# Kernel optimization log

Measured on AMD Instinct MI355X. Metric: run time of the kernel, lower is better.

Reference implementation:

```python
import jax, jax.numpy as jnp
import numpy as np

ALPHA = 0.2  # LeakyReLU negative slope
NEG_INF = -9e15


def _xavier(key, shape, gain=1.414):
    fan_in, fan_out = shape[-2], shape[-1]
    lim = gain * np.sqrt(6.0 / (fan_in + fan_out))
    return jax.random.uniform(key, shape, jnp.float32, -lim, lim)


def setup_inputs() -> dict:
    key = jax.random.key(0)
    ks = jax.random.split(key, 8)
    B, N, Din, H, Dh, Do = 8, 1024, 256, 4, 128, 64
    x = jax.random.normal(ks[0], (B, N, Din), jnp.float32)
    adj = jax.random.randint(ks[1], (B, N, N), 0, 2).astype(jnp.int32)
    W_heads = _xavier(ks[2], (H, Din, Dh))                 # per-head W
    a_heads = _xavier(ks[3], (H, 2 * Dh, 1))[..., 0]       # per-head a, [H, 2*Dh]
    W_out = _xavier(ks[4], (H * Dh, Do))                   # out_att W
    a_out = _xavier(ks[5], (2 * Do, 1))[..., 0]            # out_att a, [2*Do]
    Wf = _xavier(ks[6], (Do, Do), gain=1.0)                # fc_out linear
    bf = jnp.zeros((Do,), jnp.float32)
    return {"x": x, "adj": adj, "W_heads": W_heads, "a_heads": a_heads,
            "W_out": W_out, "a_out": a_out, "Wf": Wf, "bf": bf}


def _leaky_relu(v):
    return jnp.where(v >= 0, v, ALPHA * v)


def _gat(h, adj, W, a):
    # h: [B,N,Fin], adj: [B,N,N], W: [Fin,Fout], a: [2*Fout]
    Wh = h @ W                                   # [B,N,F]
    F = W.shape[-1]
    # additive attention: e_ij = leakyrelu(a_src.Wh_i + a_dst.Wh_j)
    src = Wh @ a[:F]                             # [B,N]
    dst = Wh @ a[F:]                             # [B,N]
    e = _leaky_relu(src[:, :, None] + dst[:, None, :])   # [B,N,N]
    scores = jnp.where(adj > 0, e, NEG_INF)
    attn = jax.nn.softmax(scores, axis=-1)       # dropout is a no-op in eval
    return attn @ Wh                             # [B,N,F]


def reference(x, adj, W_heads, a_heads, W_out, a_out, Wf, bf):
    B, N, _ = x.shape
    H, _, Dh = W_heads.shape
    # multi-head GAT, heads vmapped over leading axis of W_heads / a_heads
    heads = jax.vmap(_gat, in_axes=(None, None, 0, 0))(x, adj, W_heads, a_heads)  # [H,B,N,Dh]
    xcat = jnp.moveaxis(heads, 0, 2).reshape(B, N, H * Dh)   # concat heads, dim=2
    out = jax.nn.elu(_gat(xcat, adj, W_out, a_out))           # [B,N,Do]
    out = jax.nn.relu(out @ Wf + bf)                          # fc_out (dropout no-op)
    return out
```

## Files before the change

kernel.cpp:

```cpp
#include <hip/hip_runtime.h>
#include <hip/hip_bf16.h>

#define BSZ 8
#define NN 1024
#define DIN 256
#define NH 4
#define DH 128
#define DOUT 64
#define RTOT (BSZ*NN)
#define FCAT (NH*DH)
#define ALPHA 0.2f

typedef unsigned short ushortT;
typedef __attribute__((ext_vector_type(8))) short bf16x8;
typedef __attribute__((ext_vector_type(4))) float f32x4;

static __device__ __forceinline__ ushortT f2bf(float f) {
    __hip_bfloat16 h = __float2bfloat16(f);
    return *reinterpret_cast<ushortT*>(&h);
}
static __device__ __forceinline__ float bfu2f(ushortT u) {
    return __uint_as_float(((unsigned)u) << 16);
}
static __device__ __forceinline__ void split2(float v, ushortT& hi, ushortT& lo) {
    hi = f2bf(v);
    lo = f2bf(v - bfu2f(hi));
}
static __device__ __forceinline__ void gload16(const ushortT* g, ushortT* l) {
    __builtin_amdgcn_global_load_lds(
        (const __attribute__((address_space(1))) unsigned int*)(const void*)g,
        (__attribute__((address_space(3))) unsigned int*)(void*)l, 16, 0, 0);
}

__global__ __launch_bounds__(256) void k_prepw(const float* __restrict__ W,
                                               const float* __restrict__ Wout,
                                               ushortT* __restrict__ WbTh, ushortT* __restrict__ WbTl,
                                               ushortT* __restrict__ WoTh, ushortT* __restrict__ WoTl) {
    const int g2 = blockIdx.x * 256 + threadIdx.x;
    if (g2 < NH * DH * DIN) {
        const int h = g2 >> 15, f = (g2 >> 8) & 127, k = g2 & 255;
        const int kt = k >> 6, k64 = k & 63;
        const float v = W[(size_t)h * DIN * DH + (size_t)k * DH + f];
        ushortT hi, lo; split2(v, hi, lo);
        const int idx = ((h * 4 + kt) * 128 + f) * 64 + k64;
        WbTh[idx] = hi; WbTl[idx] = lo;
    } else {
        const int g3 = g2 - NH * DH * DIN;
        const int f = g3 >> 9, k = g3 & 511;
        const float v = Wout[(size_t)k * DOUT + f];
        ushortT hi, lo; split2(v, hi, lo);
        WoTh[g3] = hi; WoTl[g3] = lo;
    }
}

__global__ __launch_bounds__(512) void k_main(const float* __restrict__ x,
                                              const float* __restrict__ ah_,
                                              const ushortT* __restrict__ WbTh,
                                              const ushortT* __restrict__ WbTl,
                                              const int* __restrict__ adj,
                                              unsigned* __restrict__ adjbit,
                                              ushortT* __restrict__ WhT,
                                              float* __restrict__ src1,
                                              float* __restrict__ dst1) {
    __shared__ ushortT Ah[128 * 64], Al[128 * 64];
    __shared__ ushortT Bh[128 * 64], Bl[128 * 64];
    __shared__ float sred[8][32], dred[8][32];
    const int tid = threadIdx.x;
    if (blockIdx.x >= 256) {
        const int g = (blockIdx.x - 256) * 512 + tid;
        const int row = g >> 5, w = g & 31;
        const int4* p = (const int4*)(adj + (size_t)row * NN + w * 32);
        unsigned m = 0;
#pragma unroll
        for (int q = 0; q < 8; ++q) {
            const int4 v = p[q];
            m |= (v.x > 0 ? 1u : 0u) << (q * 4 + 0);
            m |= (v.y > 0 ? 1u : 0u) << (q * 4 + 1);
            m |= (v.z > 0 ? 1u : 0u) << (q * 4 + 2);
            m |= (v.w > 0 ? 1u : 0u) << (q * 4 + 3);
        }
        adjbit[g] = m;
        return;
    }
    const int lane = tid & 63, wave = tid >> 6;
    const int h = blockIdx.x >> 6, mt = blockIdx.x & 63;
    const int r0 = mt * 128, b = r0 >> 10, jr = r0 & 1023;
    const int m16 = lane & 15, quad = lane >> 4;
    const int mg = wave >> 1, fg = wave & 1;
    const int arow = tid >> 2, apart = tid & 3;
    f32x4 acc[2][4];
#pragma unroll
    for (int a = 0; a < 2; ++a)
#pragma unroll
        for (int c = 0; c < 4; ++c) acc[a][c] = (f32x4){0.f, 0.f, 0.f, 0.f};

    for (int kt = 0; kt < 4; ++kt) {
        __syncthreads();
        const ushortT* planeH = WbTh + (size_t)((h * 4 + kt) * 128) * 64;
        const ushortT* planeL = WbTl + (size_t)((h * 4 + kt) * 128) * 64;
#pragma unroll
        for (int half = 0; half < 2; ++half) {
            const int f = wave * 16 + half * 8 + (lane >> 3);
            const int sc = (lane & 7) ^ (f & 7);
            gload16(planeH + (size_t)f * 64 + sc * 8, Bh + (wave * 16 + half * 8) * 64);
            gload16(planeL + (size_t)f * 64 + sc * 8, Bl + (wave * 16 + half * 8) * 64);
        }
        {
            const float4* xs = (const float4*)(x + (size_t)(r0 + arow) * DIN + kt * 64 + apart * 16);
            union { ushortT u[16]; uint4 q[2]; } th, tl;
#pragma unroll
            for (int e = 0; e < 4; ++e) {
                const float4 v = xs[e];
                split2(v.x, th.u[e * 4 + 0], tl.u[e * 4 + 0]);
                split2(v.y, th.u[e * 4 + 1], tl.u[e * 4 + 1]);
                split2(v.z, th.u[e * 4 + 2], tl.u[e * 4 + 2]);
                split2(v.w, th.u[e * 4 + 3], tl.u[e * 4 + 3]);
            }
            const int s0 = (2 * apart) ^ (arow & 7), s1 = (2 * apart + 1) ^ (arow & 7);
            *(uint4*)&Ah[arow * 64 + s0 * 8] = th.q[0];
            *(uint4*)&Ah[arow * 64 + s1 * 8] = th.q[1];
            *(uint4*)&Al[arow * 64 + s0 * 8] = tl.q[0];
            *(uint4*)&Al[arow * 64 + s1 * 8] = tl.q[1];
        }
        __syncthreads();
#pragma unroll
        for (int ks = 0; ks < 2; ++ks) {
            bf16x8 a_h[2], a_l[2], b_h[4], b_l[4];
#pragma unroll
            for (int ms = 0; ms < 2; ++ms) {
                const int row = (mg * 2 + ms) * 16 + m16;
                const int cl = (ks * 4 + quad) ^ (row & 7);
                a_h[ms] = *(const bf16x8*)&Ah[row * 64 + cl * 8];
                a_l[ms] = *(const bf16x8*)&Al[row * 64 + cl * 8];
            }
#pragma unroll
            for (int fs = 0; fs < 4; ++fs) {
                const int row = (fg * 4 + fs) * 16 + m16;
                const int cl = (ks * 4 + quad) ^ (row & 7);
                b_h[fs] = *(const bf16x8*)&Bh[row * 64 + cl * 8];
                b_l[fs] = *(const bf16x8*)&Bl[row * 64 + cl * 8];
            }
#pragma unroll
            for (int ms = 0; ms < 2; ++ms)
#pragma unroll
                for (int fs = 0; fs < 4; ++fs) {
                    acc[ms][fs] = __builtin_amdgcn_mfma_f32_16x16x32_bf16(a_h[ms], b_h[fs], acc[ms][fs], 0, 0, 0);
                    acc[ms][fs] = __builtin_amdgcn_mfma_f32_16x16x32_bf16(a_h[ms], b_l[fs], acc[ms][fs], 0, 0, 0);
                    acc[ms][fs] = __builtin_amdgcn_mfma_f32_16x16x32_bf16(a_l[ms], b_h[fs], acc[ms][fs], 0, 0, 0);
                }
        }
    }
    float sacc[2][4] = {{0,0,0,0},{0,0,0,0}}, dacc[2][4] = {{0,0,0,0},{0,0,0,0}};
#pragma unroll
    for (int ms = 0; ms < 2; ++ms)
#pragma unroll
        for (int fs = 0; fs < 4; ++fs) {
            const int fl = (fg * 4 + fs) * 16 + m16;
            const float a_s = ah_[h * 2 * DH + fl];
            const float a_d = ah_[h * 2 * DH + DH + fl];
            union { ushortT u[4]; uint2 q; } tw;
#pragma unroll
            for (int reg = 0; reg < 4; ++reg) {
                const float v = acc[ms][fs][reg];
                sacc[ms][reg] += v * a_s;
                dacc[ms][reg] += v * a_d;
                tw.u[reg] = f2bf(v);
            }
            *(uint2*)(WhT + ((size_t)((b * NH + h) * DH + fl)) * NN + jr + (mg * 2 + ms) * 16 + quad * 4) = tw.q;
        }
#pragma unroll
    for (int ms = 0; ms < 2; ++ms) {
#pragma unroll
        for (int reg = 0; reg < 4; ++reg) {
            float s = sacc[ms][reg], d = dacc[ms][reg];
#pragma unroll
            for (int o = 8; o > 0; o >>= 1) {
                s += __shfl_xor(s, o, 64);
                d += __shfl_xor(d, o, 64);
            }
            if (m16 == 0) {
                sred[wave][ms * 16 + quad * 4 + reg] = s;
                dred[wave][ms * 16 + quad * 4 + reg] = d;
            }
        }
    }
    __syncthreads();
    if (tid < 128) {
        const int mgr = tid >> 5, idx = tid & 31;
        src1[h * RTOT + r0 + tid] = sred[mgr * 2][idx] + sred[mgr * 2 + 1][idx];
        dst1[h * RTOT + r0 + tid] = dred[mgr * 2][idx] + dred[mgr * 2 + 1][idx];
    }
}

__global__ __launch_bounds__(256) void k_attn1(const unsigned* __restrict__ adjbit,
                                               const ushortT* __restrict__ WhT,
                                               const float* __restrict__ src1,
                                               const float* __restrict__ dst1,
                                               ushortT* __restrict__ xcat) {
    __shared__ ushortT As[32 * 64];
    __shared__ ushortT Bs[128 * 64];
    __shared__ unsigned maskS[32 * 32];
    __shared__ float dstv[NN];
    __shared__ float srcv[32], rowinv[32], red4[4];
    const int tid = threadIdx.x, lane = tid & 63, wave = tid >> 6;
    const int bh = blockIdx.x & 31, it = blockIdx.x >> 5;
    const int b = bh >> 2, h = bh & 3;
    const int i0 = it * 32;
    const int m16 = lane & 15, quad = lane >> 4;

    const unsigned* mbase = adjbit + (size_t)(b * NN + i0) * 32;
#pragma unroll
    for (int k2 = 0; k2 < 4; ++k2) maskS[tid + 256 * k2] = mbase[tid + 256 * k2];
    float lm = -INFINITY;
#pragma unroll
    for (int k2 = 0; k2 < 4; ++k2) {
        const float d = dst1[h * RTOT + b * NN + tid + 256 * k2];
        dstv[tid + 256 * k2] = d;
        lm = fmaxf(lm, d);
    }
    if (tid < 32) srcv[tid] = src1[h * RTOT + b * NN + i0 + tid];
#pragma unroll
    for (int o = 32; o > 0; o >>= 1) lm = fmaxf(lm, __shfl_xor(lm, o, 64));
    if (lane == 0) red4[wave] = lm;
    __syncthreads();
    const float dmax = fmaxf(fmaxf(red4[0], red4[1]), fmaxf(red4[2], red4[3]));

    const int arow = tid >> 3, apart = tid & 7;
    const float si = srcv[arow];
    float mrow = si + dmax;
    mrow = mrow >= 0.f ? mrow : ALPHA * mrow;
    float fsum = 0.f;

    const ushortT* Bbase = WhT + (size_t)(bh * DH) * NN;
    f32x4 acc[2][2];
#pragma unroll
    for (int a = 0; a < 2; ++a)
#pragma unroll
        for (int c = 0; c < 2; ++c) acc[a][c] = (f32x4){0.f, 0.f, 0.f, 0.f};

    for (int kt = 0; kt < 16; ++kt) {
        __syncthreads();
#pragma unroll
        for (int half = 0; half < 4; ++half) {
            const int f = wave * 32 + half * 8 + (lane >> 3);
            gload16(Bbase + (size_t)f * NN + kt * 64 + (((lane & 7) ^ (f & 7)) * 8),
                    Bs + (wave * 32 + half * 8) * 64);
        }
        {
            const unsigned w0 = maskS[arow * 32 + kt * 2 + (apart >> 2)];
            const int bb = (apart & 3) * 8;
            union { ushortT u[8]; uint4 q; } tw;
#pragma unroll
            for (int e4 = 0; e4 < 2; ++e4) {
                const float4 dv = *(const float4*)&dstv[kt * 64 + apart * 8 + e4 * 4];
                const float vv[4] = {dv.x, dv.y, dv.z, dv.w};
#pragma unroll
                for (int e = 0; e < 4; ++e) {
                    float v = si + vv[e];
                    v = v >= 0.f ? v : ALPHA * v;
                    const unsigned bit = (w0 >> (bb + e4 * 4 + e)) & 1u;
                    const float p = bit ? __expf(v - mrow) : 0.f;
                    fsum += p;
                    tw.u[e4 * 4 + e] = f2bf(p);
                }
            }
            *(uint4*)&As[arow * 64 + (apart ^ (arow & 7)) * 8] = tw.q;
        }
        __syncthreads();
#pragma unroll
        for (int ks = 0; ks < 2; ++ks) {
            bf16x8 afr[2];
#pragma unroll
            for (int ms = 0; ms < 2; ++ms) {
                const int rowa = ms * 16 + m16;
                const int cla = (ks * 4 + quad) ^ (rowa & 7);
                afr[ms] = *(const bf16x8*)&As[rowa * 64 + cla * 8];
            }
#pragma unroll
            for (int ff = 0; ff < 2; ++ff) {
                const int rowb = wave * 32 + ff * 16 + m16;
                const int clb = (ks * 4 + quad) ^ (rowb & 7);
                const bf16x8 bfr = *(const bf16x8*)&Bs[rowb * 64 + clb * 8];
#pragma unroll
                for (int ms = 0; ms < 2; ++ms)
                    acc[ms][ff] = __builtin_amdgcn_mfma_f32_16x16x32_bf16(afr[ms], bfr, acc[ms][ff], 0, 0, 0);
            }
        }
    }
#pragma unroll
    for (int o = 1; o < 8; o <<= 1) fsum += __shfl_xor(fsum, o, 64);
    if ((lane & 7) == 0) rowinv[arow] = 1.f / fsum;
    __syncthreads();
#pragma unroll
    for (int ms = 0; ms < 2; ++ms) {
        float rv[4];
#pragma unroll
        for (int reg = 0; reg < 4; ++reg) rv[reg] = rowinv[ms * 16 + quad * 4 + reg];
#pragma unroll
        for (int ff = 0; ff < 2; ++ff) {
            const int f = h * DH + wave * 32 + ff * 16 + m16;
#pragma unroll
            for (int reg = 0; reg < 4; ++reg) {
                const int i = i0 + ms * 16 + quad * 4 + reg;
                xcat[(size_t)(b * NN + i) * FCAT + f] = f2bf(acc[ms][ff][reg] * rv[reg]);
            }
        }
    }
}

__global__ __launch_bounds__(256) void k_wh2(const ushortT* __restrict__ xcat,
                                             const ushortT* __restrict__ WoTh,
                                             const ushortT* __restrict__ WoTl,
                                             const float* __restrict__ aout,
                                             ushortT* __restrict__ Wh2T,
                                             float* __restrict__ src2,
                                             float* __restrict__ dst2) {
    __shared__ ushortT As[32 * 64];
    __shared__ ushortT Bh[64 * 64], Bl[64 * 64];
    __shared__ float sred[4][16], dred[4][16];
    const int tid = threadIdx.x, lane = tid & 63, wave = tid >> 6;
    const int r0 = blockIdx.x * 32;
    const int b = r0 >> 10, jr = r0 & 1023;
    const int m16 = lane & 15, quad = lane >> 4;
    const int mg = wave >> 1, fg = wave & 1;
    f32x4 acc[2] = {(f32x4){0.f,0.f,0.f,0.f}, (f32x4){0.f,0.f,0.f,0.f}};

    for (int kt = 0; kt < 8; ++kt) {
        __syncthreads();
        {
            const int row = wave * 8 + (lane >> 3);
            const int sc = (lane & 7) ^ (row & 7);
            gload16(xcat + (size_t)(r0 + row) * FCAT + kt * 64 + sc * 8, As + wave * 8 * 64);
        }
#pragma unroll
        for (int half = 0; half < 2; ++half) {
            const int f = wave * 16 + half * 8 + (lane >> 3);
            const int sc = (lane & 7) ^ (f & 7);
            gload16(WoTh + (size_t)f * FCAT + kt * 64 + sc * 8, Bh + (wave * 16 + half * 8) * 64);
            gload16(WoTl + (size_t)f * FCAT + kt * 64 + sc * 8, Bl + (wave * 16 + half * 8) * 64);
        }
        __syncthreads();
#pragma unroll
        for (int ks = 0; ks < 2; ++ks) {
            const int rowa = mg * 16 + m16;
            const int cla = (ks * 4 + quad) ^ (rowa & 7);
            const bf16x8 afr = *(const bf16x8*)&As[rowa * 64 + cla * 8];
#pragma unroll
            for (int ff = 0; ff < 2; ++ff) {
                const int rowb = fg * 32 + ff * 16 + m16;
                const int clb = (ks * 4 + quad) ^ (rowb & 7);
                const bf16x8 b_h = *(const bf16x8*)&Bh[rowb * 64 + clb * 8];
                const bf16x8 b_l = *(const bf16x8*)&Bl[rowb * 64 + clb * 8];
                acc[ff] = __builtin_amdgcn_mfma_f32_16x16x32_bf16(afr, b_h, acc[ff], 0, 0, 0);
                acc[ff] = __builtin_amdgcn_mfma_f32_16x16x32_bf16(afr, b_l, acc[ff], 0, 0, 0);
            }
        }
    }
    float sv[4] = {0, 0, 0, 0}, dv[4] = {0, 0, 0, 0};
#pragma unroll
    for (int ff = 0; ff < 2; ++ff) {
        const int f = fg * 32 + ff * 16 + m16;
        const float a_s = aout[f], a_d = aout[DOUT + f];
        union { ushortT u[4]; uint2 q; } tw;
#pragma unroll
        for (int reg = 0; reg < 4; ++reg) {
            const float v = acc[ff][reg];
            sv[reg] += v * a_s;
            dv[reg] += v * a_d;
            tw.u[reg] = f2bf(v);
        }
        *(uint2*)(Wh2T + ((size_t)(b * DOUT + f)) * NN + jr + mg * 16 + quad * 4) = tw.q;
    }
#pragma unroll
    for (int reg = 0; reg < 4; ++reg) {
#pragma unroll
        for (int o = 8; o > 0; o >>= 1) {
            sv[reg] += __shfl_xor(sv[reg], o, 64);
            dv[reg] += __shfl_xor(dv[reg], o, 64);
        }
        if (m16 == 0) { sred[wave][quad * 4 + reg] = sv[reg]; dred[wave][quad * 4 + reg] = dv[reg]; }
    }
    __syncthreads();
    if (tid < 32) {
        const int mgr = tid >> 4, idx = tid & 15;
        src2[r0 + tid] = sred[mgr * 2][idx] + sred[mgr * 2 + 1][idx];
        dst2[r0 + tid] = dred[mgr * 2][idx] + dred[mgr * 2 + 1][idx];
    }
}

__global__ __launch_bounds__(256) void k_attn2(const unsigned* __restrict__ adjbit,
                                               const ushortT* __restrict__ Wh2T,
                                               const float* __restrict__ src2,
                                               const float* __restrict__ dst2,
                                               const float* __restrict__ Wf,
                                               const float* __restrict__ bfv,
                                               float* __restrict__ out) {
    __shared__ ushortT As[32 * 64];
    __shared__ ushortT Bs[64 * 64];
    __shared__ unsigned maskS[32 * 32];
    __shared__ float dstv[NN];
    __shared__ ushortT Wfh[64 * 64], Wfl[64 * 64];
    __shared__ float t2s[32 * 68];
    __shared__ float srcv[32], rowinv[32], red4[4];
    const int tid = threadIdx.x, lane = tid & 63, wave = tid >> 6;
    const int b = blockIdx.x & 7, it = blockIdx.x >> 3;
    const int i0 = it * 32;
    const int m16 = lane & 15, quad = lane >> 4;

    const unsigned* mbase = adjbit + (size_t)(b * NN + i0) * 32;
#pragma unroll
    for (int k2 = 0; k2 < 4; ++k2) maskS[tid + 256 * k2] = mbase[tid + 256 * k2];
    float lm = -INFINITY;
#pragma unroll
    for (int k2 = 0; k2 < 4; ++k2) {
        const float d = dst2[b * NN + tid + 256 * k2];
        dstv[tid + 256 * k2] = d;
        lm = fmaxf(lm, d);
    }
    if (tid < 32) srcv[tid] = src2[b * NN + i0 + tid];
    {
        const int c = tid & 63, kc = (tid >> 6) * 16;
        union { ushortT u[16]; uint4 q[2]; } th, tl;
#pragma unroll
        for (int e = 0; e < 16; ++e)
            split2(Wf[(size_t)(kc + e) * DOUT + c], th.u[e], tl.u[e]);
        const int s0 = ((tid >> 6) * 2) ^ (c & 7), s1 = ((tid >> 6) * 2 + 1) ^ (c & 7);
        *(uint4*)&Wfh[c * 64 + s0 * 8] = th.q[0];
        *(uint4*)&Wfh[c * 64 + s1 * 8] = th.q[1];
        *(uint4*)&Wfl[c * 64 + s0 * 8] = tl.q[0];
        *(uint4*)&Wfl[c * 64 + s1 * 8] = tl.q[1];
    }
#pragma unroll
    for (int o = 32; o > 0; o >>= 1) lm = fmaxf(lm, __shfl_xor(lm, o, 64));
    if (lane == 0) red4[wave] = lm;
    __syncthreads();
    const float dmax = fmaxf(fmaxf(red4[0], red4[1]), fmaxf(red4[2], red4[3]));

    const int arow = tid >> 3, apart = tid & 7;
    const float si = srcv[arow];
    float mrow = si + dmax;
    mrow = mrow >= 0.f ? mrow : ALPHA * mrow;
    float fsum = 0.f;

    const int mfrag = wave >> 1, fh = wave & 1;
    const ushortT* Bbase = Wh2T + (size_t)(b * DOUT) * NN;
    f32x4 acc[2] = {(f32x4){0.f,0.f,0.f,0.f}, (f32x4){0.f,0.f,0.f,0.f}};

    for (int kt = 0; kt < 16; ++kt) {
        __syncthreads();
#pragma unroll
        for (int half = 0; half < 2; ++half) {
            const int f = wave * 16 + half * 8 + (lane >> 3);
            gload16(Bbase + (size_t)f * NN + kt * 64 + (((lane & 7) ^ (f & 7)) * 8),
                    Bs + (wave * 16 + half * 8) * 64);
        }
        {
            const unsigned w0 = maskS[arow * 32 + kt * 2 + (apart >> 2)];
            const int bb = (apart & 3) * 8;
            union { ushortT u[8]; uint4 q; } tw;
#pragma unroll
            for (int e4 = 0; e4 < 2; ++e4) {
                const float4 dv = *(const float4*)&dstv[kt * 64 + apart * 8 + e4 * 4];
                const float vv[4] = {dv.x, dv.y, dv.z, dv.w};
#pragma unroll
                for (int e = 0; e < 4; ++e) {
                    float v = si + vv[e];
                    v = v >= 0.f ? v : ALPHA * v;
                    const unsigned bit = (w0 >> (bb + e4 * 4 + e)) & 1u;
                    const float p = bit ? __expf(v - mrow) : 0.f;
                    fsum += p;
                    tw.u[e4 * 4 + e] = f2bf(p);
                }
            }
            *(uint4*)&As[arow * 64 + (apart ^ (arow & 7)) * 8] = tw.q;
        }
        __syncthreads();
#pragma unroll
        for (int ks = 0; ks < 2; ++ks) {
            const int rowa = mfrag * 16 + m16;
            const int cla = (ks * 4 + quad) ^ (rowa & 7);
            const bf16x8 afr = *(const bf16x8*)&As[rowa * 64 + cla * 8];
#pragma unroll
            for (int ff = 0; ff < 2; ++ff) {
                const int rowb = (fh * 2 + ff) * 16 + m16;
                const int clb = (ks * 4 + quad) ^ (rowb & 7);
                const bf16x8 bfr = *(const bf16x8*)&Bs[rowb * 64 + clb * 8];
                acc[ff] = __builtin_amdgcn_mfma_f32_16x16x32_bf16(afr, bfr, acc[ff], 0, 0, 0);
            }
        }
    }
#pragma unroll
    for (int o = 1; o < 8; o <<= 1) fsum += __shfl_xor(fsum, o, 64);
    if ((lane & 7) == 0) rowinv[arow] = 1.f / fsum;
    __syncthreads();
#pragma unroll
    for (int ff = 0; ff < 2; ++ff) {
#pragma unroll
        for (int reg = 0; reg < 4; ++reg) {
            const int row = mfrag * 16 + quad * 4 + reg;
            float v = acc[ff][reg] * rowinv[row];
            v = v > 0.f ? v : (__expf(v) - 1.f);
            t2s[row * 68 + (fh * 2 + ff) * 16 + m16] = v;
        }
    }
    __syncthreads();
    const int mf = wave >> 1, nh = wave & 1;
    f32x4 oacc[2];
#pragma unroll
    for (int g = 0; g < 2; ++g) {
        const float bias = bfv[(nh * 2 + g) * 16 + m16];
        oacc[g] = (f32x4){bias, bias, bias, bias};
    }
#pragma unroll
    for (int ks = 0; ks < 2; ++ks) {
        const int rowa = mf * 16 + m16;
        const float4 fA = *(const float4*)&t2s[rowa * 68 + ks * 32 + quad * 8];
        const float4 fB = *(const float4*)&t2s[rowa * 68 + ks * 32 + quad * 8 + 4];
        union { ushortT u[8]; bf16x8 v; } a_h, a_l;
        const float av[8] = {fA.x, fA.y, fA.z, fA.w, fB.x, fB.y, fB.z, fB.w};
#pragma unroll
        for (int e = 0; e < 8; ++e) split2(av[e], a_h.u[e], a_l.u[e]);
#pragma unroll
        for (int g = 0; g < 2; ++g) {
            const int rowc = (nh * 2 + g) * 16 + m16;
            const int cl = (ks * 4 + quad) ^ (rowc & 7);
            const bf16x8 b_h = *(const bf16x8*)&Wfh[rowc * 64 + cl * 8];
            const bf16x8 b_l = *(const bf16x8*)&Wfl[rowc * 64 + cl * 8];
            oacc[g] = __builtin_amdgcn_mfma_f32_16x16x32_bf16(a_h.v, b_h, oacc[g], 0, 0, 0);
            oacc[g] = __builtin_amdgcn_mfma_f32_16x16x32_bf16(a_h.v, b_l, oacc[g], 0, 0, 0);
            oacc[g] = __builtin_amdgcn_mfma_f32_16x16x32_bf16(a_l.v, b_h, oacc[g], 0, 0, 0);
        }
    }
#pragma unroll
    for (int g = 0; g < 2; ++g) {
        const int c = (nh * 2 + g) * 16 + m16;
#pragma unroll
        for (int reg = 0; reg < 4; ++reg) {
            const int i = i0 + mf * 16 + quad * 4 + reg;
            out[(size_t)(b * NN + i) * DOUT + c] = fmaxf(oacc[g][reg], 0.f);
        }
    }
}

extern "C" void kernel_launch(void* const* d_in, const int* in_sizes, int n_in,
                              void* d_out, int out_size, void* d_ws, size_t ws_size,
                              hipStream_t stream) {
    const float* x   = (const float*)d_in[0];
    const int*   adj = (const int*)d_in[1];
    const float* Wh  = (const float*)d_in[2];
    const float* ah  = (const float*)d_in[3];
    const float* Wo  = (const float*)d_in[4];
    const float* ao  = (const float*)d_in[5];
    const float* Wf  = (const float*)d_in[6];
    const float* bf  = (const float*)d_in[7];
    float* out = (float*)d_out;

    float* ws    = (float*)d_ws;
    float* src1  = ws;
    float* dst1  = src1 + NH * RTOT;
    float* src2  = dst1 + NH * RTOT;
    float* dst2  = src2 + RTOT;
    ushortT* WhT   = (ushortT*)(dst2 + RTOT);
    ushortT* Wh2T  = WhT + (size_t)RTOT * FCAT;
    ushortT* xcat  = Wh2T + (size_t)RTOT * DOUT;
    ushortT* WbTh  = xcat + (size_t)RTOT * FCAT;
    ushortT* WbTl  = WbTh + NH * DH * DIN;
    ushortT* WoTh  = WbTl + NH * DH * DIN;
    ushortT* WoTl  = WoTh + DOUT * FCAT;
    unsigned* adjbit = (unsigned*)(WoTl + DOUT * FCAT);

    hipLaunchKernelGGL(k_prepw, dim3((NH * DH * DIN + DOUT * FCAT) / 256), dim3(256), 0, stream,
                       Wh, Wo, WbTh, WbTl, WoTh, WoTl);
    hipLaunchKernelGGL(k_main,  dim3(768), dim3(512), 0, stream,
                       x, ah, WbTh, WbTl, adj, adjbit, WhT, src1, dst1);
    hipLaunchKernelGGL(k_attn1, dim3(1024), dim3(256), 0, stream,
                       adjbit, WhT, src1, dst1, xcat);
    hipLaunchKernelGGL(k_wh2,   dim3(256), dim3(256), 0, stream,
                       xcat, WoTh, WoTl, ao, Wh2T, src2, dst2);
    hipLaunchKernelGGL(k_attn2, dim3(256), dim3(256), 0, stream,
                       adjbit, Wh2T, src2, dst2, Wf, bf, out);
}
```

Baseline: 158.6 us.

## Double-buffer attention tiles in k_attn1 to overlap staging with MFMA

Doubles the As and Bs shared-memory tiles in the first-layer attention kernel. The next tile's attention weights and WhT slice are now staged while the current tile runs its MFMAs, with one barrier per iteration instead of two. This aims to hide global-load latency and the exp/mask arithmetic behind matrix work. In exchange, LDS use per block roughly doubles for these tiles, which may lower occupancy. Correctness depends on the barrier also waiting for the asynchronous loads to finish.

```diff
diff --git a/kernel.cpp b/kernel.cpp
--- a/kernel.cpp
+++ b/kernel.cpp
@@ -197,8 +197,8 @@
                                                const float* __restrict__ src1,
                                                const float* __restrict__ dst1,
                                                ushortT* __restrict__ xcat) {
-    __shared__ ushortT As[32 * 64];
-    __shared__ ushortT Bs[128 * 64];
+    __shared__ ushortT As[2][32 * 64];
+    __shared__ ushortT Bs[2][128 * 64];
     __shared__ unsigned maskS[32 * 32];
     __shared__ float dstv[NN];
     __shared__ float srcv[32], rowinv[32], red4[4];
@@ -238,35 +238,41 @@
 #pragma unroll
         for (int c = 0; c < 2; ++c) acc[a][c] = (f32x4){0.f, 0.f, 0.f, 0.f};
 
+#define STAGE_TILE(kt_, buf_)                                                              \
+    {                                                                                      \
+        const int kt__ = (kt_);                                                            \
+        ushortT* bdst = &Bs[(buf_)][0];                                                    \
+        _Pragma("unroll")                                                                  \
+        for (int half = 0; half < 4; ++half) {                                             \
+            const int f = wave * 32 + half * 8 + (lane >> 3);                              \
+            gload16(Bbase + (size_t)f * NN + kt__ * 64 + (((lane & 7) ^ (f & 7)) * 8),     \
+                    bdst + (wave * 32 + half * 8) * 64);                                   \
+        }                                                                                  \
+        const unsigned w0 = maskS[arow * 32 + kt__ * 2 + (apart >> 2)];                    \
+        const int bb = (apart & 3) * 8;                                                    \
+        union { ushortT u[8]; uint4 q; } tw;                                               \
+        _Pragma("unroll")                                                                  \
+        for (int e4 = 0; e4 < 2; ++e4) {                                                   \
+            const float4 dv = *(const float4*)&dstv[kt__ * 64 + apart * 8 + e4 * 4];       \
+            const float vv[4] = {dv.x, dv.y, dv.z, dv.w};                                  \
+            _Pragma("unroll")                                                              \
+            for (int e = 0; e < 4; ++e) {                                                  \
+                float v = si + vv[e];                                                      \
+                v = v >= 0.f ? v : ALPHA * v;                                              \
+                const unsigned bit = (w0 >> (bb + e4 * 4 + e)) & 1u;                       \
+                const float p = bit ? __expf(v - mrow) : 0.f;                              \
+                fsum += p;                                                                 \
+                tw.u[e4 * 4 + e] = f2bf(p);                                                \
+            }                                                                              \
+        }                                                                                  \
+        *(uint4*)&As[(buf_)][arow * 64 + (apart ^ (arow & 7)) * 8] = tw.q;                 \
+    }
+
+    STAGE_TILE(0, 0);
     for (int kt = 0; kt < 16; ++kt) {
-        __syncthreads();
-#pragma unroll
-        for (int half = 0; half < 4; ++half) {
-            const int f = wave * 32 + half * 8 + (lane >> 3);
-            gload16(Bbase + (size_t)f * NN + kt * 64 + (((lane & 7) ^ (f & 7)) * 8),
-                    Bs + (wave * 32 + half * 8) * 64);
-        }
-        {
-            const unsigned w0 = maskS[arow * 32 + kt * 2 + (apart >> 2)];
-            const int bb = (apart & 3) * 8;
-            union { ushortT u[8]; uint4 q; } tw;
-#pragma unroll
-            for (int e4 = 0; e4 < 2; ++e4) {
-                const float4 dv = *(const float4*)&dstv[kt * 64 + apart * 8 + e4 * 4];
-                const float vv[4] = {dv.x, dv.y, dv.z, dv.w};
-#pragma unroll
-                for (int e = 0; e < 4; ++e) {
-                    float v = si + vv[e];
-                    v = v >= 0.f ? v : ALPHA * v;
-                    const unsigned bit = (w0 >> (bb + e4 * 4 + e)) & 1u;
-                    const float p = bit ? __expf(v - mrow) : 0.f;
-                    fsum += p;
-                    tw.u[e4 * 4 + e] = f2bf(p);
-                }
-            }
-            *(uint4*)&As[arow * 64 + (apart ^ (arow & 7)) * 8] = tw.q;
-        }
-        __syncthreads();
+        const int cb = kt & 1;
+        __syncthreads();
+        if (kt < 15) STAGE_TILE(kt + 1, cb ^ 1);
 #pragma unroll
         for (int ks = 0; ks < 2; ++ks) {
             bf16x8 afr[2];
@@ -274,19 +280,20 @@
             for (int ms = 0; ms < 2; ++ms) {
                 const int rowa = ms * 16 + m16;
                 const int cla = (ks * 4 + quad) ^ (rowa & 7);
-                afr[ms] = *(const bf16x8*)&As[rowa * 64 + cla * 8];
+                afr[ms] = *(const bf16x8*)&As[cb][rowa * 64 + cla * 8];
             }
 #pragma unroll
             for (int ff = 0; ff < 2; ++ff) {
                 const int rowb = wave * 32 + ff * 16 + m16;
                 const int clb = (ks * 4 + quad) ^ (rowb & 7);
-                const bf16x8 bfr = *(const bf16x8*)&Bs[rowb * 64 + clb * 8];
+                const bf16x8 bfr = *(const bf16x8*)&Bs[cb][rowb * 64 + clb * 8];
 #pragma unroll
                 for (int ms = 0; ms < 2; ++ms)
                     acc[ms][ff] = __builtin_amdgcn_mfma_f32_16x16x32_bf16(afr[ms], bfr, acc[ms][ff], 0, 0, 0);
             }
         }
     }
+#undef STAGE_TILE
 #pragma unroll
     for (int o = 1; o < 8; o <<= 1) fsum += __shfl_xor(fsum, o, 64);
     if ((lane & 7) == 0) rowinv[arow] = 1.f / fsum;
```

New measurement: 155.6 us (median of 2 runs). No clear change (-1.9%).

## Compute attention probabilities directly in MFMA A-fragment registers, drop LDS staging

Applied to the files above, without the earlier changes.

Each wave now owns 16 rows and 64 features, and builds its bf16 probability A-fragment in registers in the exact MFMA lane layout. This removes the As shared buffer, its store/load round trip, and the rowinv/srcv shared arrays; row sums are reduced with lane shuffles. In exchange, each exp is now computed by two waves (the 2 feature-half waves share rows), doubling exp work per block.

```diff
diff --git a/kernel.cpp b/kernel.cpp
--- a/kernel.cpp
+++ b/kernel.cpp
@@ -197,16 +197,16 @@
                                                const float* __restrict__ src1,
                                                const float* __restrict__ dst1,
                                                ushortT* __restrict__ xcat) {
-    __shared__ ushortT As[32 * 64];
     __shared__ ushortT Bs[128 * 64];
     __shared__ unsigned maskS[32 * 32];
     __shared__ float dstv[NN];
-    __shared__ float srcv[32], rowinv[32], red4[4];
+    __shared__ float red4[4];
     const int tid = threadIdx.x, lane = tid & 63, wave = tid >> 6;
     const int bh = blockIdx.x & 31, it = blockIdx.x >> 5;
     const int b = bh >> 2, h = bh & 3;
     const int i0 = it * 32;
     const int m16 = lane & 15, quad = lane >> 4;
+    const int rw = wave >> 1, fw = wave & 1;
 
     const unsigned* mbase = adjbit + (size_t)(b * NN + i0) * 32;
 #pragma unroll
@@ -218,25 +218,22 @@
         dstv[tid + 256 * k2] = d;
         lm = fmaxf(lm, d);
     }
-    if (tid < 32) srcv[tid] = src1[h * RTOT + b * NN + i0 + tid];
 #pragma unroll
     for (int o = 32; o > 0; o >>= 1) lm = fmaxf(lm, __shfl_xor(lm, o, 64));
     if (lane == 0) red4[wave] = lm;
     __syncthreads();
     const float dmax = fmaxf(fmaxf(red4[0], red4[1]), fmaxf(red4[2], red4[3]));
 
-    const int arow = tid >> 3, apart = tid & 7;
-    const float si = srcv[arow];
+    const int rloc = rw * 16 + m16;
+    const float si = src1[h * RTOT + b * NN + i0 + rloc];
     float mrow = si + dmax;
     mrow = mrow >= 0.f ? mrow : ALPHA * mrow;
     float fsum = 0.f;
 
     const ushortT* Bbase = WhT + (size_t)(bh * DH) * NN;
-    f32x4 acc[2][2];
-#pragma unroll
-    for (int a = 0; a < 2; ++a)
-#pragma unroll
-        for (int c = 0; c < 2; ++c) acc[a][c] = (f32x4){0.f, 0.f, 0.f, 0.f};
+    f32x4 acc[4];
+#pragma unroll
+    for (int c = 0; c < 4; ++c) acc[c] = (f32x4){0.f, 0.f, 0.f, 0.f};
 
     for (int kt = 0; kt < 16; ++kt) {
         __syncthreads();
@@ -246,64 +243,52 @@
             gload16(Bbase + (size_t)f * NN + kt * 64 + (((lane & 7) ^ (f & 7)) * 8),
                     Bs + (wave * 32 + half * 8) * 64);
         }
-        {
-            const unsigned w0 = maskS[arow * 32 + kt * 2 + (apart >> 2)];
-            const int bb = (apart & 3) * 8;
-            union { ushortT u[8]; uint4 q; } tw;
+        bf16x8 av[2];
+#pragma unroll
+        for (int ks = 0; ks < 2; ++ks) {
+            const unsigned w0 = maskS[rloc * 32 + kt * 2 + ks];
+            union { ushortT u[8]; bf16x8 v; } ta;
 #pragma unroll
             for (int e4 = 0; e4 < 2; ++e4) {
-                const float4 dv = *(const float4*)&dstv[kt * 64 + apart * 8 + e4 * 4];
+                const float4 dv = *(const float4*)&dstv[kt * 64 + ks * 32 + quad * 8 + e4 * 4];
                 const float vv[4] = {dv.x, dv.y, dv.z, dv.w};
 #pragma unroll
                 for (int e = 0; e < 4; ++e) {
                     float v = si + vv[e];
                     v = v >= 0.f ? v : ALPHA * v;
-                    const unsigned bit = (w0 >> (bb + e4 * 4 + e)) & 1u;
+                    const unsigned bit = (w0 >> (quad * 8 + e4 * 4 + e)) & 1u;
                     const float p = bit ? __expf(v - mrow) : 0.f;
                     fsum += p;
-                    tw.u[e4 * 4 + e] = f2bf(p);
+                    ta.u[e4 * 4 + e] = f2bf(p);
                 }
             }
-            *(uint4*)&As[arow * 64 + (apart ^ (arow & 7)) * 8] = tw.q;
+            av[ks] = ta.v;
         }
         __syncthreads();
 #pragma unroll
         for (int ks = 0; ks < 2; ++ks) {
-            bf16x8 afr[2];
-#pragma unroll
-            for (int ms = 0; ms < 2; ++ms) {
-                const int rowa = ms * 16 + m16;
-                const int cla = (ks * 4 + quad) ^ (rowa & 7);
-                afr[ms] = *(const bf16x8*)&As[rowa * 64 + cla * 8];
-            }
-#pragma unroll
-            for (int ff = 0; ff < 2; ++ff) {
-                const int rowb = wave * 32 + ff * 16 + m16;
+#pragma unroll
+            for (int ff = 0; ff < 4; ++ff) {
+                const int rowb = fw * 64 + ff * 16 + m16;
                 const int clb = (ks * 4 + quad) ^ (rowb & 7);
                 const bf16x8 bfr = *(const bf16x8*)&Bs[rowb * 64 + clb * 8];
-#pragma unroll
-                for (int ms = 0; ms < 2; ++ms)
-                    acc[ms][ff] = __builtin_amdgcn_mfma_f32_16x16x32_bf16(afr[ms], bfr, acc[ms][ff], 0, 0, 0);
-            }
-        }
-    }
-#pragma unroll
-    for (int o = 1; o < 8; o <<= 1) fsum += __shfl_xor(fsum, o, 64);
-    if ((lane & 7) == 0) rowinv[arow] = 1.f / fsum;
-    __syncthreads();
-#pragma unroll
-    for (int ms = 0; ms < 2; ++ms) {
-        float rv[4];
-#pragma unroll
-        for (int reg = 0; reg < 4; ++reg) rv[reg] = rowinv[ms * 16 + quad * 4 + reg];
-#pragma unroll
-        for (int ff = 0; ff < 2; ++ff) {
-            const int f = h * DH + wave * 32 + ff * 16 + m16;
-#pragma unroll
-            for (int reg = 0; reg < 4; ++reg) {
-                const int i = i0 + ms * 16 + quad * 4 + reg;
-                xcat[(size_t)(b * NN + i) * FCAT + f] = f2bf(acc[ms][ff][reg] * rv[reg]);
-            }
+                acc[ff] = __builtin_amdgcn_mfma_f32_16x16x32_bf16(av[ks], bfr, acc[ff], 0, 0, 0);
+            }
+        }
+    }
+    fsum += __shfl_xor(fsum, 16, 64);
+    fsum += __shfl_xor(fsum, 32, 64);
+    const float inv = 1.f / fsum;
+    float rv[4];
+#pragma unroll
+    for (int reg = 0; reg < 4; ++reg) rv[reg] = __shfl(inv, quad * 4 + reg, 64);
+#pragma unroll
+    for (int ff = 0; ff < 4; ++ff) {
+        const int f = h * DH + fw * 64 + ff * 16 + m16;
+#pragma unroll
+        for (int reg = 0; reg < 4; ++reg) {
+            const int i = i0 + rw * 16 + quad * 4 + reg;
+            xcat[(size_t)(b * NN + i) * FCAT + f] = f2bf(acc[ff][reg] * rv[reg]);
         }
     }
 }
```

After: 156.4 us. About the same (-1.4%).
